# Kernel tuning notes

Hardware: AMD Instinct MI355X
Metric: run time of the kernel (lower is better)

Reference implementation:

```python
import jax, jax.numpy as jnp
import numpy as np

B, S, D, H = 16, 1024, 768, 12
HD = D // H  # head_dim = 64


def setup_inputs() -> dict:
    key = jax.random.key(0)
    k1, k2, k3 = jax.random.split(key, 3)
    x = jax.random.normal(k1, (B, S, D), dtype=jnp.float32)
    # torch Linear default init ~ U(-1/sqrt(in), 1/sqrt(in)); use small normal for stability
    W_qkv = jax.random.normal(k2, (D, 3 * D), dtype=jnp.float32) * 0.02
    b_qkv = jnp.zeros((3 * D,), dtype=jnp.float32)
    W_out = jax.random.normal(k3, (D, D), dtype=jnp.float32) * 0.02
    b_out = jnp.zeros((D,), dtype=jnp.float32)
    return {"x": x, "W_qkv": W_qkv, "b_qkv": b_qkv, "W_out": W_out, "b_out": b_out, "mode": 0}


def reference(x, W_qkv, b_qkv, W_out, b_out, mode):
    # x: [B, S, D]; mode is unused (dropout is identity in eval)
    b, s, d = x.shape
    qkv = x @ W_qkv + b_qkv                                   # [B, S, 3D]
    qkv = qkv.reshape(b, s, 3, H, HD).transpose(2, 0, 3, 1, 4)  # [3, B, H, S, HD]
    Q, K, V = qkv[0], qkv[1], qkv[2]
    # NOTE: original has NO softmax and NO 1/sqrt(d) scale — pure matmul chain
    scores = jnp.einsum("bhsd,bhtd->bhst", Q, K)              # [B, H, S, S]
    out = jnp.einsum("bhst,bhtd->bhsd", scores, V)            # [B, H, S, HD]
    out = out.transpose(0, 2, 1, 3).reshape(b, s, d)          # [B, S, D]
    return out @ W_out + b_out
```

## Files before the change

### kernel.cpp

```cpp
#include <hip/hip_runtime.h>
#include <hip/hip_bf16.h>


typedef __attribute__((ext_vector_type(8))) short bf16x8;
typedef __attribute__((ext_vector_type(4))) short short4v;
typedef __attribute__((ext_vector_type(4))) float f32x4;
typedef __attribute__((ext_vector_type(4))) float float4v;

typedef __attribute__((address_space(1))) const unsigned char ga_u8;
typedef __attribute__((address_space(3))) unsigned char la_u8;

__device__ __forceinline__ unsigned short f2bf(float f) {
  union { float f; unsigned int u; } v; v.f = f;
  unsigned int u = v.u;
  return (unsigned short)((u + 0x7FFFu + ((u >> 16) & 1u)) >> 16);
}

__global__ __launch_bounds__(256) void prologue(const float* __restrict__ x,
                                                unsigned short* __restrict__ xbf,
                                                const float* __restrict__ Wqkv,
                                                unsigned short* __restrict__ WqkvT,
                                                const float* __restrict__ Wout,
                                                unsigned short* __restrict__ WoutT) {
  __shared__ unsigned short tile[32][33];
  const int blk = blockIdx.x;
  if (blk < 6144) {
    const long long i = (long long)(blk * 256 + threadIdx.x) * 8;
    float4v v0 = *(const float4v*)(x + i);
    float4v v1 = *(const float4v*)(x + i + 4);
    bf16x8 o;
    o[0] = (short)f2bf(v0[0]); o[1] = (short)f2bf(v0[1]);
    o[2] = (short)f2bf(v0[2]); o[3] = (short)f2bf(v0[3]);
    o[4] = (short)f2bf(v1[0]); o[5] = (short)f2bf(v1[1]);
    o[6] = (short)f2bf(v1[2]); o[7] = (short)f2bf(v1[3]);
    *(bf16x8*)(xbf + i) = o;
    return;
  }
  const float* in;
  unsigned short* out;
  int bx, by, C;
  if (blk < 7872) {
    const int bb = blk - 6144;
    in = Wqkv; out = WqkvT; C = 2304;
    bx = (bb % 72) * 32; by = (bb / 72) * 32;
  } else {
    const int bb = blk - 7872;
    in = Wout; out = WoutT; C = 768;
    bx = (bb % 24) * 32; by = (bb / 24) * 32;
  }
  const int R = 768;
  const int tx = threadIdx.x & 31, ty = threadIdx.x >> 5;
  #pragma unroll
  for (int i = 0; i < 32; i += 8)
    tile[ty + i][tx] = f2bf(in[(long long)(by + ty + i) * C + bx + tx]);
  __syncthreads();
  #pragma unroll
  for (int i = 0; i < 32; i += 8)
    out[(long long)(bx + ty + i) * R + by + tx] = tile[tx][ty + i];
}

struct GemmArgs {
  const void* A;
  const unsigned short* BT;
  void* C;
  unsigned short* KT;
  unsigned short* VT;
  const float* bias;
  int K;
  int lda, ldbt, ldc;
  long long sA1, sB1, sC1;
};


#define MFMA_(a, b, c) __builtin_amdgcn_mfma_f32_16x16x32_bf16(a, b, c, 0, 0, 0)
#define TBV { asm volatile("s_waitcnt vmcnt(3)" ::: "memory");                 \
              __builtin_amdgcn_s_barrier(); asm volatile("" ::: "memory"); }

#define RD_HALF(dstA, dstB, bc, br, LOF)                                       \
  {                                                                            \
    const unsigned short* As_ = &L[(bc) * 16384 + wmA];                        \
    const unsigned short* Bs_ = &L[32768 + (br) * 12288 + wnB];                \
    _Pragma("unroll")                                                          \
    for (int x = 0; x < 3; ++x) dstB[x] = *(const bf16x8*)&Bs_[x * 1024 + LOF];\
    _Pragma("unroll")                                                          \
    for (int x = 0; x < 8; ++x) dstA[x] = *(const bf16x8*)&As_[x * 1024 + LOF];\
  }

template <int OMODE>
__global__ __launch_bounds__(512, 2) void gemm1b(GemmArgs g) {
  __shared__ unsigned short L[69632];

  const int gx = gridDim.x, gy = gridDim.y;
  const int nwg = gx * gy * gridDim.z;
  int flat = (blockIdx.z * gy + blockIdx.y) * gx + blockIdx.x;
  flat = (flat & 7) * (nwg >> 3) + (flat >> 3);
  const int gxy = gx * gy;
  const int bz = flat / gxy;
  const int rem = flat - bz * gxy;
  const int by = rem / gx;
  const int bx = rem - by * gx;

  const long long offA = bz * g.sA1;
  const long long offB = bz * g.sB1;
  const long long offC = bz * g.sC1;
  const int bm = by * 256, bn = bx * 192;

  const int tid = threadIdx.x;
  const int lane = tid & 63, wave = tid >> 6;
  const int wm = wave >> 2, wn = wave & 3;
  const int l15 = lane & 15, l4 = lane >> 4;

  const int lof0 = l15 * 64 + (((l4 + l15) * 8) & 63);
  const int lof1 = l15 * 64 + ((32 + (l4 + l15) * 8) & 63);
  const int wmA = wm * 8192;
  const int wnB = wn * 3072;

  int LA[4], DA[4], LB[3], DB[3];
  #pragma unroll
  for (int r = 0; r < 4; ++r) {
    const int c = tid + r * 512;
    const int row = c >> 3, j = c & 7;
    LA[r] = row * g.lda + ((j - row) & 7) * 8;
    DA[r] = c * 8;
  }
  #pragma unroll
  for (int r = 0; r < 3; ++r) {
    const int c = tid + r * 512;
    const int row = c >> 3, j = c & 7;
    LB[r] = row * g.ldbt + ((j - row) & 7) * 8;
    DB[r] = c * 8;
  }

  const unsigned short* Ab = (const unsigned short*)g.A + offA + (long long)bm * g.lda;
  const unsigned short* Bb = g.BT + offB + (long long)bn * g.ldbt;

  auto stA = [&](int bufsel, const unsigned short* p) {
    unsigned short* dst = &L[bufsel * 16384];
    #pragma unroll
    for (int r = 0; r < 4; ++r)
      __builtin_amdgcn_global_load_lds((ga_u8*)(p + LA[r]), (la_u8*)(dst + DA[r]), 16, 0, 0);
  };
  auto stB = [&](int bb, const unsigned short* p) {
    unsigned short* dst = &L[32768 + bb * 12288];
    #pragma unroll
    for (int r = 0; r < 3; ++r)
      __builtin_amdgcn_global_load_lds((ga_u8*)(p + LB[r]), (la_u8*)(dst + DB[r]), 16, 0, 0);
  };

  const f32x4 fz = {0.f, 0.f, 0.f, 0.f};
  f32x4 acc[8][3];
  #pragma unroll
  for (int i = 0; i < 8; ++i)
    #pragma unroll
    for (int j = 0; j < 3; ++j) acc[i][j] = fz;

  const unsigned short* pA = Ab;
  const unsigned short* pB = Bb;

  stA(0, pA); pA += 64;
  stB(0, pB); pB += 64;
  stB(1, pB); pB += 64;
  TBV

  bf16x8 af0[8], bf0[3], af1[8], bf1[3];
  int bufc = 0, bbr = 0, bbs = 2;
  RD_HALF(af0, bf0, 0, 0, lof0)

  const int NT = g.K >> 6;
  for (int t = 0; t < NT; ++t) {
    RD_HALF(af1, bf1, bufc, bbr, lof1)
    stA(bufc ^ 1, pA); pA += 64;
    stB(bbs, pB); pB += 64;

    __builtin_amdgcn_s_setprio(1);
    #pragma unroll
    for (int nf = 0; nf < 3; ++nf)
      #pragma unroll
      for (int rj = 0; rj < 8; ++rj)
        acc[rj][nf] = MFMA_(af0[rj], bf0[nf], acc[rj][nf]);
    #pragma unroll
    for (int nf = 0; nf < 3; ++nf)
      #pragma unroll
      for (int rj = 0; rj < 8; ++rj)
        acc[rj][nf] = MFMA_(af1[rj], bf1[nf], acc[rj][nf]);
    __builtin_amdgcn_s_setprio(0);

    TBV
    bufc ^= 1;
    bbr = (bbr == 2) ? 0 : bbr + 1;
    bbs = (bbs == 2) ? 0 : bbs + 1;
    RD_HALF(af0, bf0, bufc, bbr, lof0)
  }

  const int row0 = bm + wm * 128 + l4 * 4;
  const int col0 = wn * 48 + l15;
  if (OMODE == 2) {
    #pragma unroll
    for (int mf = 0; mf < 8; ++mf)
      #pragma unroll
      for (int nf = 0; nf < 3; ++nf) {
        const int col = bn + col0 + nf * 16;
        const float bv = g.bias[col];
        #pragma unroll
        for (int ii = 0; ii < 4; ++ii)
          ((float*)g.C)[offC + (long long)(row0 + mf * 16 + ii) * g.ldc + col] =
              acc[mf][nf][ii] + bv;
      }
  } else if (bn < 768) {
    #pragma unroll
    for (int mf = 0; mf < 8; ++mf)
      #pragma unroll
      for (int nf = 0; nf < 3; ++nf) {
        const int col = bn + col0 + nf * 16;
        const float bv = g.bias[col];
        #pragma unroll
        for (int ii = 0; ii < 4; ++ii)
          ((unsigned short*)g.C)[(long long)(row0 + mf * 16 + ii) * 768 + col] =
              f2bf(acc[mf][nf][ii] + bv);
      }
  } else {
    unsigned short* T = (bn < 1536) ? g.KT : g.VT;
    const int rbase = (bn < 1536) ? 768 : 1536;
    const int b = bm >> 10;
    const int t0 = (row0 & 1023);
    #pragma unroll
    for (int nf = 0; nf < 3; ++nf) {
      const int gcol = bn + col0 + nf * 16;
      const float bv = g.bias[gcol];
      const int cr = gcol - rbase;
      const int h = cr >> 6, d = cr & 63;
      unsigned short* Tb = T + ((long long)(b * 12 + h) * 64 + d) * 1024;
      #pragma unroll
      for (int mf = 0; mf < 8; ++mf) {
        short4v sv;
        #pragma unroll
        for (int ii = 0; ii < 4; ++ii) sv[ii] = (short)f2bf(acc[mf][nf][ii] + bv);
        *(short4v*)&Tb[t0 + mf * 16] = sv;
      }
    }
  }
}

__global__ __launch_bounds__(256) void ktv_mfma(const unsigned short* __restrict__ KT,
                                                const unsigned short* __restrict__ VT,
                                                unsigned short* __restrict__ Mh) {
  __shared__ unsigned short L[2][2][4096];
  const int z = blockIdx.x;
  const int tid = threadIdx.x;
  const int lane = tid & 63, wave = tid >> 6;
  const int l15 = lane & 15, l4 = lane >> 4;

  const int lof0 = l15 * 64 + (((l4 + l15) * 8) & 63);
  const int lof1 = l15 * 64 + ((32 + (l4 + l15) * 8) & 63);

  int LS[2], DS[2];
  #pragma unroll
  for (int r = 0; r < 2; ++r) {
    const int c = tid + r * 256;
    const int row = c >> 3, j = c & 7;
    LS[r] = row * 1024 + ((j - row) & 7) * 8;
    DS[r] = c * 8;
  }
  const unsigned short* Ab = KT + (long long)z * 65536;
  const unsigned short* Bb = VT + (long long)z * 65536;

  auto stg = [&](int buf, const unsigned short* pa, const unsigned short* pb) {
    #pragma unroll
    for (int r = 0; r < 2; ++r) {
      __builtin_amdgcn_global_load_lds((ga_u8*)(pa + LS[r]), (la_u8*)(&L[buf][0][0] + DS[r]), 16, 0, 0);
      __builtin_amdgcn_global_load_lds((ga_u8*)(pb + LS[r]), (la_u8*)(&L[buf][1][0] + DS[r]), 16, 0, 0);
    }
  };

  const f32x4 fz = {0.f, 0.f, 0.f, 0.f};
  f32x4 acc[4];
  #pragma unroll
  for (int i = 0; i < 4; ++i) acc[i] = fz;

  const int eb = wave * 1024;
  stg(0, Ab, Bb);
  for (int t = 0; t < 16; ++t) {
    asm volatile("s_waitcnt vmcnt(0)" ::: "memory");
    __builtin_amdgcn_s_barrier();
    asm volatile("" ::: "memory");
    const int buf = t & 1;
    bf16x8 bv0 = *(const bf16x8*)&L[buf][1][eb + lof0];
    bf16x8 bv1 = *(const bf16x8*)&L[buf][1][eb + lof1];
    bf16x8 a0[4], a1[4];
    #pragma unroll
    for (int mf = 0; mf < 4; ++mf) {
      a0[mf] = *(const bf16x8*)&L[buf][0][mf * 1024 + lof0];
      a1[mf] = *(const bf16x8*)&L[buf][0][mf * 1024 + lof1];
    }
    if (t < 15) stg(buf ^ 1, Ab + (t + 1) * 64, Bb + (t + 1) * 64);
    #pragma unroll
    for (int mf = 0; mf < 4; ++mf) acc[mf] = MFMA_(a0[mf], bv0, acc[mf]);
    #pragma unroll
    for (int mf = 0; mf < 4; ++mf) acc[mf] = MFMA_(a1[mf], bv1, acc[mf]);
    __builtin_amdgcn_s_barrier();
    asm volatile("" ::: "memory");
  }

  unsigned short* mb = Mh + (long long)z * 4096;
  const int e = wave * 16 + l15;
  #pragma unroll
  for (int mf = 0; mf < 4; ++mf)
    #pragma unroll
    for (int ii = 0; ii < 4; ++ii)
      mb[(mf * 16 + l4 * 4 + ii) * 64 + e] = f2bf(acc[mf][ii]);
}

__global__ __launch_bounds__(256) void gemm_w2t(const unsigned short* __restrict__ WoutT,
                                                const unsigned short* __restrict__ Mh,
                                                unsigned short* __restrict__ W2T) {
  constexpr int LDT = 72;
  __shared__ unsigned short As[128 * LDT];
  __shared__ unsigned short Bs[64 * LDT];

  const int bm = blockIdx.x * 128;
  const int z = blockIdx.y;
  const int b = z / 12, h = z % 12;
  const int tid = threadIdx.x;
  const int lane = tid & 63, wave = tid >> 6;
  const int l15 = lane & 15, l4 = lane >> 4;
  const int srow = tid >> 3, scg = (tid & 7) * 8;

  const unsigned short* Abase = WoutT + (long long)bm * 768 + h * 64;
  #pragma unroll
  for (int s = 0; s < 4; ++s) {
    const int row = s * 32 + srow;
    *(bf16x8*)&As[row * LDT + scg] =
        *(const bf16x8*)(Abase + (long long)row * 768 + scg);
  }
  #pragma unroll
  for (int s = 0; s < 2; ++s) {
    const int row = s * 32 + srow;
    *(bf16x8*)&Bs[row * LDT + scg] =
        *(const bf16x8*)(Mh + (long long)z * 4096 + row * 64 + scg);
  }
  __syncthreads();

  const f32x4 fz = {0.f, 0.f, 0.f, 0.f};
  f32x4 acc[2][4];
  #pragma unroll
  for (int i = 0; i < 2; ++i)
    #pragma unroll
    for (int j = 0; j < 4; ++j) acc[i][j] = fz;

  #pragma unroll
  for (int ks = 0; ks < 64; ks += 32) {
    const int kk = ks + l4 * 8;
    bf16x8 af[2], bfv[4];
    #pragma unroll
    for (int i = 0; i < 2; ++i)
      af[i] = *(const bf16x8*)&As[(wave * 32 + i * 16 + l15) * LDT + kk];
    #pragma unroll
    for (int i = 0; i < 4; ++i)
      bfv[i] = *(const bf16x8*)&Bs[(i * 16 + l15) * LDT + kk];
    #pragma unroll
    for (int mi = 0; mi < 2; ++mi)
      #pragma unroll
      for (int ni = 0; ni < 4; ++ni)
        acc[mi][ni] = MFMA_(af[mi], bfv[ni], acc[mi][ni]);
  }

  unsigned short* Cb = W2T + (long long)b * 589824 + h * 64;
  #pragma unroll
  for (int mi = 0; mi < 2; ++mi)
    #pragma unroll
    for (int ni = 0; ni < 4; ++ni)
      #pragma unroll
      for (int ii = 0; ii < 4; ++ii) {
        const int row = bm + wave * 32 + mi * 16 + l4 * 4 + ii;
        const int col = ni * 16 + l15;
        Cb[(long long)row * 768 + col] = f2bf(acc[mi][ni][ii]);
      }
}

extern "C" void kernel_launch(void* const* d_in, const int* in_sizes, int n_in,
                              void* d_out, int out_size, void* d_ws, size_t ws_size,
                              hipStream_t stream) {
  (void)in_sizes; (void)n_in; (void)out_size; (void)ws_size;
  const float* x    = (const float*)d_in[0];
  const float* Wqkv = (const float*)d_in[1];
  const float* bqkv = (const float*)d_in[2];
  const float* Wout = (const float*)d_in[3];
  const float* bout = (const float*)d_in[4];
  float* out = (float*)d_out;

  char* ws = (char*)d_ws;
  size_t off = 0;
  auto carve = [&](size_t bytes) {
    char* p = ws + off;
    off += (bytes + 255) & ~(size_t)255;
    return p;
  };
  unsigned short* WqkvT = (unsigned short*)carve((size_t)2304 * 768 * 2);
  unsigned short* WoutT = (unsigned short*)carve((size_t)768 * 768 * 2);
  unsigned short* Qbuf  = (unsigned short*)carve((size_t)16384 * 768 * 2);
  unsigned short* KT    = (unsigned short*)carve((size_t)192 * 64 * 1024 * 2);
  unsigned short* VT    = (unsigned short*)carve((size_t)192 * 64 * 1024 * 2);
  unsigned short* Mh    = (unsigned short*)carve((size_t)192 * 64 * 64 * 2);
  unsigned short* xbf   = (unsigned short*)carve((size_t)16384 * 768 * 2);
  unsigned short* W2T   = xbf;
  carve((size_t)1 << 18);

  prologue<<<dim3(8448), 256, 0, stream>>>(x, xbf, Wqkv, WqkvT, Wout, WoutT);

  GemmArgs g1{};
  g1.A = xbf; g1.BT = WqkvT; g1.C = Qbuf; g1.KT = KT; g1.VT = VT; g1.bias = bqkv;
  g1.K = 768; g1.lda = 768; g1.ldbt = 768; g1.ldc = 768;
  gemm1b<1><<<dim3(12, 64, 1), 512, 0, stream>>>(g1);

  ktv_mfma<<<dim3(192), 256, 0, stream>>>(KT, VT, Mh);

  gemm_w2t<<<dim3(6, 192), 256, 0, stream>>>(WoutT, Mh, W2T);

  GemmArgs g3{};
  g3.A = Qbuf; g3.BT = W2T; g3.C = out; g3.bias = bout;
  g3.K = 768; g3.lda = 768; g3.ldbt = 768; g3.ldc = 768;
  g3.sA1 = 786432;
  g3.sB1 = 589824;
  g3.sC1 = 786432;
  gemm1b<2><<<dim3(4, 4, 16), 512, 0, stream>>>(g3);
}
```

Before: 129.7 us.

## Fuse fp32-to-bf16 conversion of x into QKV GEMM and triple-buffer ktv

Removes the separate pass that converted x to bf16. The QKV GEMM now loads fp32 x directly into registers, converts it, and writes bf16 into LDS, software-pipelined two K-tiles ahead with register double buffers. This avoids writing and re-reading a 25 MB bf16 copy of x, but it replaces async global-to-LDS loads for the A operand with register loads, which raises register pressure and adds conversion ALU work inside the GEMM loop. Separately, ktv_mfma moves from double to triple buffering with a relaxed vmcnt wait so that loads run further ahead of the MFMAs.

```diff
diff --git a/kernel.cpp b/kernel.cpp
--- a/kernel.cpp
+++ b/kernel.cpp
@@ -16,35 +16,20 @@
   return (unsigned short)((u + 0x7FFFu + ((u >> 16) & 1u)) >> 16);
 }
 
-__global__ __launch_bounds__(256) void prologue(const float* __restrict__ x,
-                                                unsigned short* __restrict__ xbf,
-                                                const float* __restrict__ Wqkv,
+__global__ __launch_bounds__(256) void prologue(const float* __restrict__ Wqkv,
                                                 unsigned short* __restrict__ WqkvT,
                                                 const float* __restrict__ Wout,
                                                 unsigned short* __restrict__ WoutT) {
   __shared__ unsigned short tile[32][33];
   const int blk = blockIdx.x;
-  if (blk < 6144) {
-    const long long i = (long long)(blk * 256 + threadIdx.x) * 8;
-    float4v v0 = *(const float4v*)(x + i);
-    float4v v1 = *(const float4v*)(x + i + 4);
-    bf16x8 o;
-    o[0] = (short)f2bf(v0[0]); o[1] = (short)f2bf(v0[1]);
-    o[2] = (short)f2bf(v0[2]); o[3] = (short)f2bf(v0[3]);
-    o[4] = (short)f2bf(v1[0]); o[5] = (short)f2bf(v1[1]);
-    o[6] = (short)f2bf(v1[2]); o[7] = (short)f2bf(v1[3]);
-    *(bf16x8*)(xbf + i) = o;
-    return;
-  }
   const float* in;
   unsigned short* out;
   int bx, by, C;
-  if (blk < 7872) {
-    const int bb = blk - 6144;
+  if (blk < 1728) {
     in = Wqkv; out = WqkvT; C = 2304;
-    bx = (bb % 72) * 32; by = (bb / 72) * 32;
+    bx = (blk % 72) * 32; by = (blk / 72) * 32;
   } else {
-    const int bb = blk - 7872;
+    const int bb = blk - 1728;
     in = Wout; out = WoutT; C = 768;
     bx = (bb % 24) * 32; by = (bb / 24) * 32;
   }
@@ -73,8 +58,11 @@
 
 
 #define MFMA_(a, b, c) __builtin_amdgcn_mfma_f32_16x16x32_bf16(a, b, c, 0, 0, 0)
-#define TBV { asm volatile("s_waitcnt vmcnt(3)" ::: "memory");                 \
-              __builtin_amdgcn_s_barrier(); asm volatile("" ::: "memory"); }
+#define INC3(v) ((v) == 2 ? 0 : (v) + 1)
+#define TBV3  { asm volatile("s_waitcnt vmcnt(3)" ::: "memory");               \
+                __builtin_amdgcn_s_barrier(); asm volatile("" ::: "memory"); }
+#define TBV11 { asm volatile("s_waitcnt vmcnt(11) lgkmcnt(0)" ::: "memory");   \
+                __builtin_amdgcn_s_barrier(); asm volatile("" ::: "memory"); }
 
 #define RD_HALF(dstA, dstB, bc, br, LOF)                                       \
   {                                                                            \
@@ -84,6 +72,44 @@
     for (int x = 0; x < 3; ++x) dstB[x] = *(const bf16x8*)&Bs_[x * 1024 + LOF];\
     _Pragma("unroll")                                                          \
     for (int x = 0; x < 8; ++x) dstA[x] = *(const bf16x8*)&As_[x * 1024 + LOF];\
+  }
+
+#define MFMA_TILE                                                              \
+  {                                                                            \
+    __builtin_amdgcn_s_setprio(1);                                             \
+    _Pragma("unroll")                                                          \
+    for (int nf = 0; nf < 3; ++nf)                                             \
+      _Pragma("unroll")                                                        \
+      for (int rj = 0; rj < 8; ++rj)                                           \
+        acc[rj][nf] = MFMA_(af0[rj], bf0[nf], acc[rj][nf]);                    \
+    _Pragma("unroll")                                                          \
+    for (int nf = 0; nf < 3; ++nf)                                             \
+      _Pragma("unroll")                                                        \
+      for (int rj = 0; rj < 8; ++rj)                                           \
+        acc[rj][nf] = MFMA_(af1[rj], bf1[nf], acc[rj][nf]);                    \
+    __builtin_amdgcn_s_setprio(0);                                             \
+  }
+
+#define LOADF(f, p)                                                            \
+  {                                                                            \
+    _Pragma("unroll")                                                          \
+    for (int r = 0; r < 4; ++r) {                                              \
+      f[r][0] = *(const float4v*)((p) + LA[r]);                                \
+      f[r][1] = *(const float4v*)((p) + LA[r] + 4);                            \
+    }                                                                          \
+  }
+
+#define CVTW(f, bufsel)                                                        \
+  {                                                                            \
+    _Pragma("unroll")                                                          \
+    for (int r = 0; r < 4; ++r) {                                              \
+      bf16x8 o;                                                                \
+      _Pragma("unroll")                                                        \
+      for (int v = 0; v < 4; ++v) o[v] = (short)f2bf(f[r][0][v]);              \
+      _Pragma("unroll")                                                        \
+      for (int v = 0; v < 4; ++v) o[4 + v] = (short)f2bf(f[r][1][v]);          \
+      *(bf16x8*)&L[(bufsel) * 16384 + DA[r]] = o;                              \
+    }                                                                          \
   }
 
 template <int OMODE>
@@ -131,15 +157,7 @@
     DB[r] = c * 8;
   }
 
-  const unsigned short* Ab = (const unsigned short*)g.A + offA + (long long)bm * g.lda;
   const unsigned short* Bb = g.BT + offB + (long long)bn * g.ldbt;
-
-  auto stA = [&](int bufsel, const unsigned short* p) {
-    unsigned short* dst = &L[bufsel * 16384];
-    #pragma unroll
-    for (int r = 0; r < 4; ++r)
-      __builtin_amdgcn_global_load_lds((ga_u8*)(p + LA[r]), (la_u8*)(dst + DA[r]), 16, 0, 0);
-  };
   auto stB = [&](int bb, const unsigned short* p) {
     unsigned short* dst = &L[32768 + bb * 12288];
     #pragma unroll
@@ -154,42 +172,79 @@
     #pragma unroll
     for (int j = 0; j < 3; ++j) acc[i][j] = fz;
 
-  const unsigned short* pA = Ab;
   const unsigned short* pB = Bb;
-
-  stA(0, pA); pA += 64;
-  stB(0, pB); pB += 64;
-  stB(1, pB); pB += 64;
-  TBV
-
   bf16x8 af0[8], bf0[3], af1[8], bf1[3];
-  int bufc = 0, bbr = 0, bbs = 2;
-  RD_HALF(af0, bf0, 0, 0, lof0)
-
   const int NT = g.K >> 6;
-  for (int t = 0; t < NT; ++t) {
-    RD_HALF(af1, bf1, bufc, bbr, lof1)
-    stA(bufc ^ 1, pA); pA += 64;
-    stB(bbs, pB); pB += 64;
-
-    __builtin_amdgcn_s_setprio(1);
-    #pragma unroll
-    for (int nf = 0; nf < 3; ++nf)
-      #pragma unroll
-      for (int rj = 0; rj < 8; ++rj)
-        acc[rj][nf] = MFMA_(af0[rj], bf0[nf], acc[rj][nf]);
-    #pragma unroll
-    for (int nf = 0; nf < 3; ++nf)
-      #pragma unroll
-      for (int rj = 0; rj < 8; ++rj)
-        acc[rj][nf] = MFMA_(af1[rj], bf1[nf], acc[rj][nf]);
-    __builtin_amdgcn_s_setprio(0);
-
-    TBV
-    bufc ^= 1;
-    bbr = (bbr == 2) ? 0 : bbr + 1;
-    bbs = (bbs == 2) ? 0 : bbs + 1;
-    RD_HALF(af0, bf0, bufc, bbr, lof0)
+
+  if constexpr (OMODE == 1) {
+    const float* Ab = (const float*)g.A + offA + (long long)bm * g.lda;
+    const float* pAf = Ab;
+    float4v fX[4][2], fY[4][2];
+
+    LOADF(fX, pAf); pAf += 64;
+    LOADF(fY, pAf); pAf += 64;
+    stB(0, pB); pB += 64;
+    stB(1, pB); pB += 64;
+    CVTW(fX, 0);
+    asm volatile("s_waitcnt vmcnt(3) lgkmcnt(0)" ::: "memory");
+    __builtin_amdgcn_s_barrier();
+    asm volatile("" ::: "memory");
+
+    int bbr = 0, bbs = 2;
+    RD_HALF(af0, bf0, 0, 0, lof0)
+
+    const int NP = NT >> 1;
+    for (int i = 0; i < NP; ++i) {
+      RD_HALF(af1, bf1, 0, bbr, lof1)
+      {
+        const float* s = (2 * i + 2 < NT) ? pAf : Ab;
+        LOADF(fX, s); pAf += 64;
+      }
+      stB(bbs, pB); pB += 64; bbs = INC3(bbs);
+      MFMA_TILE
+      CVTW(fY, 1)
+      TBV11
+      bbr = INC3(bbr);
+      RD_HALF(af0, bf0, 1, bbr, lof0)
+      RD_HALF(af1, bf1, 1, bbr, lof1)
+      {
+        const float* s = (2 * i + 3 < NT) ? pAf : Ab;
+        LOADF(fY, s); pAf += 64;
+      }
+      stB(bbs, pB); pB += 64; bbs = INC3(bbs);
+      MFMA_TILE
+      CVTW(fX, 0)
+      TBV11
+      bbr = INC3(bbr);
+      RD_HALF(af0, bf0, 0, bbr, lof0)
+    }
+  } else {
+    const unsigned short* Ab = (const unsigned short*)g.A + offA + (long long)bm * g.lda;
+    auto stA = [&](int bufsel, const unsigned short* p) {
+      unsigned short* dst = &L[bufsel * 16384];
+      #pragma unroll
+      for (int r = 0; r < 4; ++r)
+        __builtin_amdgcn_global_load_lds((ga_u8*)(p + LA[r]), (la_u8*)(dst + DA[r]), 16, 0, 0);
+    };
+    const unsigned short* pA = Ab;
+    stA(0, pA); pA += 64;
+    stB(0, pB); pB += 64;
+    stB(1, pB); pB += 64;
+    TBV3
+
+    int bufc = 0, bbr = 0, bbs = 2;
+    RD_HALF(af0, bf0, 0, 0, lof0)
+    for (int t = 0; t < NT; ++t) {
+      RD_HALF(af1, bf1, bufc, bbr, lof1)
+      stA(bufc ^ 1, pA); pA += 64;
+      stB(bbs, pB); pB += 64;
+      MFMA_TILE
+      TBV3
+      bufc ^= 1;
+      bbr = INC3(bbr);
+      bbs = INC3(bbs);
+      RD_HALF(af0, bf0, bufc, bbr, lof0)
+    }
   }
 
   const int row0 = bm + wm * 128 + l4 * 4;
@@ -244,7 +299,7 @@
 __global__ __launch_bounds__(256) void ktv_mfma(const unsigned short* __restrict__ KT,
                                                 const unsigned short* __restrict__ VT,
                                                 unsigned short* __restrict__ Mh) {
-  __shared__ unsigned short L[2][2][4096];
+  __shared__ unsigned short L[3][2][4096];
   const int z = blockIdx.x;
   const int tid = threadIdx.x;
   const int lane = tid & 63, wave = tid >> 6;
@@ -264,7 +319,9 @@
   const unsigned short* Ab = KT + (long long)z * 65536;
   const unsigned short* Bb = VT + (long long)z * 65536;
 
-  auto stg = [&](int buf, const unsigned short* pa, const unsigned short* pb) {
+  auto stg = [&](int buf, int t) {
+    const unsigned short* pa = Ab + t * 64;
+    const unsigned short* pb = Bb + t * 64;
     #pragma unroll
     for (int r = 0; r < 2; ++r) {
       __builtin_amdgcn_global_load_lds((ga_u8*)(pa + LS[r]), (la_u8*)(&L[buf][0][0] + DS[r]), 16, 0, 0);
@@ -278,12 +335,13 @@
   for (int i = 0; i < 4; ++i) acc[i] = fz;
 
   const int eb = wave * 1024;
-  stg(0, Ab, Bb);
+  stg(0, 0);
+  stg(1, 1);
   for (int t = 0; t < 16; ++t) {
-    asm volatile("s_waitcnt vmcnt(0)" ::: "memory");
+    asm volatile("s_waitcnt vmcnt(4)" ::: "memory");
     __builtin_amdgcn_s_barrier();
     asm volatile("" ::: "memory");
-    const int buf = t & 1;
+    const int buf = t % 3;
     bf16x8 bv0 = *(const bf16x8*)&L[buf][1][eb + lof0];
     bf16x8 bv1 = *(const bf16x8*)&L[buf][1][eb + lof1];
     bf16x8 a0[4], a1[4];
@@ -292,7 +350,7 @@
       a0[mf] = *(const bf16x8*)&L[buf][0][mf * 1024 + lof0];
       a1[mf] = *(const bf16x8*)&L[buf][0][mf * 1024 + lof1];
     }
-    if (t < 15) stg(buf ^ 1, Ab + (t + 1) * 64, Bb + (t + 1) * 64);
+    stg((t + 2) % 3, (t + 2 < 16) ? t + 2 : 0);
     #pragma unroll
     for (int mf = 0; mf < 4; ++mf) acc[mf] = MFMA_(a0[mf], bv0, acc[mf]);
     #pragma unroll
@@ -401,14 +459,13 @@
   unsigned short* KT    = (unsigned short*)carve((size_t)192 * 64 * 1024 * 2);
   unsigned short* VT    = (unsigned short*)carve((size_t)192 * 64 * 1024 * 2);
   unsigned short* Mh    = (unsigned short*)carve((size_t)192 * 64 * 64 * 2);
-  unsigned short* xbf   = (unsigned short*)carve((size_t)16384 * 768 * 2);
-  unsigned short* W2T   = xbf;
+  unsigned short* W2T   = (unsigned short*)carve((size_t)16 * 768 * 768 * 2);
   carve((size_t)1 << 18);
 
-  prologue<<<dim3(8448), 256, 0, stream>>>(x, xbf, Wqkv, WqkvT, Wout, WoutT);
+  prologue<<<dim3(2304), 256, 0, stream>>>(Wqkv, WqkvT, Wout, WoutT);
 
   GemmArgs g1{};
-  g1.A = xbf; g1.BT = WqkvT; g1.C = Qbuf; g1.KT = KT; g1.VT = VT; g1.bias = bqkv;
+  g1.A = x; g1.BT = WqkvT; g1.C = Qbuf; g1.KT = KT; g1.VT = VT; g1.bias = bqkv;
   g1.K = 768; g1.lda = 768; g1.ldbt = 768; g1.ldc = 768;
   gemm1b<1><<<dim3(12, 64, 1), 512, 0, stream>>>(g1);
 
```

Measured after the change: 266.9 us. 106% more time.
